# Performance work log

Hardware: AMD Instinct MI355X
Metric: run time of the kernel (lower is better)

The kernel has to match this reference:

```python
import jax, jax.numpy as jnp
import numpy as np

B, T, D, H = 4, 2048, 1024, 16
DH = D // H


def setup_inputs() -> dict:
    key = jax.random.key(0)
    k_x, k_qkv, k_out = jax.random.split(key, 3)
    x = jax.random.normal(k_x, (B, T, D), dtype=jnp.float32)
    padding_mask_1d = jnp.ones((B, T), dtype=bool)
    # Linear weights stored as [in, out] (torch stores [out, in]; math identical via x @ W)
    Wqkv = jax.random.normal(k_qkv, (D, 3 * D), dtype=jnp.float32) * 0.02
    bqkv = jnp.zeros((3 * D,), dtype=jnp.float32)
    Wout = jax.random.normal(k_out, (D, D), dtype=jnp.float32) * 0.02
    bout = jnp.zeros((D,), dtype=jnp.float32)
    return {"x": x, "padding_mask_1d": padding_mask_1d, "Wqkv": Wqkv,
            "bqkv": bqkv, "Wout": Wout, "bout": bout}


def reference(x, padding_mask_1d, Wqkv, bqkv, Wout, bout):
    b, t, d = x.shape
    # QKV projection
    qkv = x @ Wqkv + bqkv                      # [B,T,3D]
    q, k, v = jnp.split(qkv, 3, axis=-1)
    # split heads -> [B,H,T,Dh]
    def split_heads(u):
        return u.reshape(b, t, H, DH).transpose(0, 2, 1, 3)
    Q, K, V = split_heads(q), split_heads(k), split_heads(v)
    # scores [B,H,T,T]
    logits = jnp.einsum('bhqd,bhkd->bhqk', Q, K) / jnp.sqrt(jnp.asarray(DH, x.dtype))
    # padding mask [B,1,1,T] & causal mask [1,1,T,T]
    pad = padding_mask_1d[:, None, None, :]
    causal = jnp.tril(jnp.ones((t, t), dtype=bool))[None, None]
    mask = pad & causal
    logits = jnp.where(mask, logits, -jnp.inf)
    weights = jax.nn.softmax(logits, axis=-1)  # dropout=0.0 -> identity
    out = jnp.einsum('bhqk,bhkd->bhqd', weights, V)  # [B,H,T,Dh]
    out = out.transpose(0, 2, 1, 3).reshape(b, t, d)  # merge heads
    out = out @ Wout + bout
    return out
```

## Files before the change

### kernel.cpp

```cpp
#include <hip/hip_runtime.h>
#include <math.h>

typedef unsigned short u16;
typedef float f32x4 __attribute__((ext_vector_type(4)));
typedef short bf16x8 __attribute__((ext_vector_type(8)));

typedef const unsigned char __attribute__((address_space(1))) cu8_as1;
typedef unsigned char __attribute__((address_space(3))) u8_as3;

__device__ __forceinline__ void gload_lds16(const void* g, void* l) {
  __builtin_amdgcn_global_load_lds((cu8_as1*)g, (u8_as3*)l, 16, 0, 0);
}

__device__ __forceinline__ u16 f2b(float f) {
  union { float f; unsigned u; } v; v.f = f;
  unsigned r = v.u + 0x7FFFu + ((v.u >> 16) & 1u);
  return (u16)(r >> 16);
}

__global__ __launch_bounds__(256) void k_cvt(const float* __restrict__ in,
                                             u16* __restrict__ out, int n4) {
  int i = blockIdx.x * 256 + threadIdx.x;
  if (i >= n4) return;
  float4 v = ((const float4*)in)[i];
  ushort4 o;
  o.x = f2b(v.x); o.y = f2b(v.y); o.z = f2b(v.z); o.w = f2b(v.w);
  ((ushort4*)out)[i] = o;
}

__global__ __launch_bounds__(256) void k_transpose_cvt(const float* __restrict__ in,
                                                       u16* __restrict__ out,
                                                       int R, int C) {
  __shared__ float tile[32][33];
  int c0 = blockIdx.x * 32, r0 = blockIdx.y * 32;
  int tx = threadIdx.x, ty = threadIdx.y;
#pragma unroll
  for (int j = 0; j < 32; j += 8)
    tile[ty + j][tx] = in[(size_t)(r0 + ty + j) * C + c0 + tx];
  __syncthreads();
#pragma unroll
  for (int j = 0; j < 32; j += 8)
    out[(size_t)(c0 + ty + j) * R + r0 + tx] = f2b(tile[tx][ty + j]);
}

#define BM 128
#define BN 128
#define BKk 32

#define QSCALE 0.1803368801111244f

template <int EPI>
__global__ __launch_bounds__(256) void k_gemm_bt(
    const u16* __restrict__ A, const u16* __restrict__ Bt,
    const float* __restrict__ bias, float* __restrict__ outp,
    int M, int N, int K,
    u16* __restrict__ Qb, u16* __restrict__ Kb, u16* __restrict__ Vtb) {
  __shared__ u16 As[BM * BKk];
  __shared__ u16 Bs[BN * BKk];
  int tid = threadIdx.x;
  int lane = tid & 63, w = tid >> 6;
  int lo = lane & 15, hi = lane >> 4;
  int wr = w >> 1, wc = w & 1;
  int m0 = blockIdx.x * BM, n0 = blockIdx.y * BN;
  const u16* Ab = A + (size_t)m0 * K;
  const u16* Bb = Bt + (size_t)n0 * K;

  f32x4 acc[4][4];
#pragma unroll
  for (int i = 0; i < 4; ++i)
#pragma unroll
    for (int j = 0; j < 4; ++j) acc[i][j] = (f32x4){0.f, 0.f, 0.f, 0.f};

  for (int kt = 0; kt < K; kt += BKk) {
#pragma unroll
    for (int q = 0; q < 2; ++q) {
      int idx = q * 256 + tid;
      int row = idx >> 2, cb = idx & 3;
      gload_lds16(Ab + (size_t)row * K + kt + cb * 8, &As[idx * 8]);
      gload_lds16(Bb + (size_t)row * K + kt + cb * 8, &Bs[idx * 8]);
    }
    __syncthreads();
    bf16x8 af[4], bf[4];
#pragma unroll
    for (int i = 0; i < 4; ++i) {
      af[i] = *(const bf16x8*)&As[(wr * 64 + i * 16 + lo) * BKk + hi * 8];
      bf[i] = *(const bf16x8*)&Bs[(wc * 64 + i * 16 + lo) * BKk + hi * 8];
    }
#pragma unroll
    for (int i = 0; i < 4; ++i)
#pragma unroll
      for (int j = 0; j < 4; ++j)
        acc[i][j] = __builtin_amdgcn_mfma_f32_16x16x32_bf16(af[i], bf[j], acc[i][j], 0, 0, 0);
    __syncthreads();
  }

#pragma unroll
  for (int i = 0; i < 4; ++i) {
#pragma unroll
    for (int j = 0; j < 4; ++j) {
      int col = n0 + wc * 64 + j * 16 + lo;
      float bv = bias[col];
#pragma unroll
      for (int r = 0; r < 4; ++r) {
        int row = m0 + wr * 64 + i * 16 + hi * 4 + r;
        float v = acc[i][j][r] + bv;
        if (EPI == 1) {
          outp[(size_t)row * N + col] = v;
        } else {
          int b = row >> 11, t = row & 2047;
          int reg = col >> 10, nr = col & 1023;
          int h = nr >> 6, d = nr & 63;
          int bh = b * 16 + h;
          if (reg == 0)
            Qb[((size_t)bh * 2048 + t) * 64 + d] = f2b(v * QSCALE);
          else if (reg == 1)
            Kb[((size_t)bh * 2048 + t) * 64 + d] = f2b(v);
          else
            Vtb[((size_t)bh * 64 + d) * 2048 + t] = f2b(v);
        }
      }
    }
  }
}

#define M2FIX 8.0f

__global__ __launch_bounds__(128) void k_attn(const u16* __restrict__ Qb,
                                              const u16* __restrict__ Kb,
                                              const u16* __restrict__ Vtb,
                                              u16* __restrict__ Ob) {
  __shared__ u16 Pl[2][32 * 40];
  int lane = threadIdx.x & 63, w = threadIdx.x >> 6;
  int lo = lane & 15, hi = lane >> 4;
  int bh = blockIdx.x;
  int qt = ((gridDim.y - 1 - blockIdx.y) << 1) + w;
  int qr = qt * 32;
  const u16* Qh = Qb + (size_t)bh * 2048 * 64;
  const u16* Kh = Kb + (size_t)bh * 2048 * 64;
  const u16* Vh = Vtb + (size_t)bh * 64 * 2048;
  u16* Pw = Pl[w];

  bf16x8 qf[2][2];
#pragma unroll
  for (int m = 0; m < 2; ++m)
#pragma unroll
    for (int c = 0; c < 2; ++c)
      qf[m][c] = *(const bf16x8*)&Qh[(size_t)(qr + m * 16 + lo) * 64 + c * 32 + hi * 8];

  f32x4 o[2][4];
  float lsum[2][4];
#pragma unroll
  for (int m = 0; m < 2; ++m) {
#pragma unroll
    for (int dc = 0; dc < 4; ++dc) o[m][dc] = (f32x4){0.f, 0.f, 0.f, 0.f};
#pragma unroll
    for (int r = 0; r < 4; ++r) lsum[m][r] = 0.f;
  }

  for (int kt = 0; kt < qr + 32; kt += 32) {
    bf16x8 kf[2][2];
#pragma unroll
    for (int kc = 0; kc < 2; ++kc)
#pragma unroll
      for (int c = 0; c < 2; ++c)
        kf[kc][c] = *(const bf16x8*)&Kh[(size_t)(kt + kc * 16 + lo) * 64 + c * 32 + hi * 8];

    f32x4 s[2][2];
#pragma unroll
    for (int m = 0; m < 2; ++m)
#pragma unroll
      for (int kc = 0; kc < 2; ++kc) {
        f32x4 z = (f32x4){0.f, 0.f, 0.f, 0.f};
        z = __builtin_amdgcn_mfma_f32_16x16x32_bf16(qf[m][0], kf[kc][0], z, 0, 0, 0);
        s[m][kc] = __builtin_amdgcn_mfma_f32_16x16x32_bf16(qf[m][1], kf[kc][1], z, 0, 0, 0);
      }

    if (kt + 31 > qr) {
#pragma unroll
      for (int m = 0; m < 2; ++m)
#pragma unroll
        for (int kc = 0; kc < 2; ++kc) {
          int key = kt + kc * 16 + lo;
#pragma unroll
          for (int r = 0; r < 4; ++r) {
            int rowa = qr + m * 16 + hi * 4 + r;
            if (key > rowa) s[m][kc][r] = -INFINITY;
          }
        }
    }

#pragma unroll
    for (int m = 0; m < 2; ++m) {
#pragma unroll
      for (int kc = 0; kc < 2; ++kc)
#pragma unroll
        for (int r = 0; r < 4; ++r)
          s[m][kc][r] = __builtin_amdgcn_exp2f(s[m][kc][r] - M2FIX);
#pragma unroll
      for (int r = 0; r < 4; ++r)
        lsum[m][r] += s[m][0][r] + s[m][1][r];
#pragma unroll
      for (int kc = 0; kc < 2; ++kc)
#pragma unroll
        for (int r = 0; r < 4; ++r)
          Pw[(m * 16 + hi * 4 + r) * 40 + kc * 16 + lo] = f2b(s[m][kc][r]);
    }

    bf16x8 pa[2];
#pragma unroll
    for (int m = 0; m < 2; ++m)
      pa[m] = *(const bf16x8*)&Pw[(m * 16 + lo) * 40 + hi * 8];
    bf16x8 vf[4];
#pragma unroll
    for (int dc = 0; dc < 4; ++dc)
      vf[dc] = *(const bf16x8*)&Vh[(size_t)(dc * 16 + lo) * 2048 + kt + hi * 8];
#pragma unroll
    for (int m = 0; m < 2; ++m)
#pragma unroll
      for (int dc = 0; dc < 4; ++dc)
        o[m][dc] = __builtin_amdgcn_mfma_f32_16x16x32_bf16(pa[m], vf[dc], o[m][dc], 0, 0, 0);
  }

#pragma unroll
  for (int m = 0; m < 2; ++m)
#pragma unroll
    for (int off = 1; off < 16; off <<= 1)
#pragma unroll
      for (int r = 0; r < 4; ++r)
        lsum[m][r] += __shfl_xor(lsum[m][r], off);

  int b = bh >> 4, h = bh & 15;
#pragma unroll
  for (int m = 0; m < 2; ++m) {
    float rl[4];
#pragma unroll
    for (int r = 0; r < 4; ++r) rl[r] = 1.f / lsum[m][r];
#pragma unroll
    for (int dc = 0; dc < 4; ++dc)
#pragma unroll
      for (int r = 0; r < 4; ++r) {
        int t = qr + m * 16 + hi * 4 + r;
        int d = h * 64 + dc * 16 + lo;
        Ob[((size_t)(b * 2048 + t)) * 1024 + d] = f2b(o[m][dc][r] * rl[r]);
      }
  }
}

extern "C" void kernel_launch(void* const* d_in, const int* in_sizes, int n_in,
                              void* d_out, int out_size, void* d_ws, size_t ws_size,
                              hipStream_t stream) {
  const float* x    = (const float*)d_in[0];
  const float* Wqkv = (const float*)d_in[2];
  const float* bqkv = (const float*)d_in[3];
  const float* Wout = (const float*)d_in[4];
  const float* bout = (const float*)d_in[5];
  float* out = (float*)d_out;

  char* ws = (char*)d_ws;
  u16* xb    = (u16*)(ws);
  u16* WqkvT = (u16*)(ws + (16u << 20));
  u16* WoutT = (u16*)(ws + (22u << 20));
  u16* Qb    = (u16*)(ws + (24u << 20));
  u16* Kb    = (u16*)(ws + (40u << 20));
  u16* Vtb   = (u16*)(ws + (56u << 20));
  u16* Ob    = (u16*)(ws + (72u << 20));

  k_cvt<<<8192, 256, 0, stream>>>(x, xb, 8192 * 1024 / 4);
  k_transpose_cvt<<<dim3(96, 32), dim3(32, 8), 0, stream>>>(Wqkv, WqkvT, 1024, 3072);
  k_transpose_cvt<<<dim3(32, 32), dim3(32, 8), 0, stream>>>(Wout, WoutT, 1024, 1024);
  k_gemm_bt<0><<<dim3(64, 24), 256, 0, stream>>>(xb, WqkvT, bqkv, nullptr,
                                                 8192, 3072, 1024, Qb, Kb, Vtb);
  k_attn<<<dim3(64, 32), 128, 0, stream>>>(Qb, Kb, Vtb, Ob);
  k_gemm_bt<1><<<dim3(64, 8), 256, 0, stream>>>(Ob, WoutT, bout, out,
                                                8192, 1024, 1024, nullptr, nullptr, nullptr);
}
```

Measured before the change: 339.2 us.

## Split attention key range across two waves and combine partial outputs

Each attention block now serves a single 32-row query tile, and its two waves each process half of the causal key tiles instead of separate query tiles. The grid doubles to 64×64 blocks. Each wave writes its unnormalized bf16 partial output and row sums. A new combine kernel adds the two partials and normalizes them. Because the softmax max is fixed, no rescaling is needed when combining. The aim is shorter per-wave critical paths and better balance of the causal tail, at the cost of an extra launch, roughly 48MB of extra traffic, loading Q twice, and extra bf16 rounding of the partial sums.

Result: slower. 350.2 us (+3.2%).

```diff
diff --git a/kernel.cpp b/kernel.cpp
--- a/kernel.cpp
+++ b/kernel.cpp
@@ -16,6 +16,11 @@
   union { float f; unsigned u; } v; v.f = f;
   unsigned r = v.u + 0x7FFFu + ((v.u >> 16) & 1u);
   return (u16)(r >> 16);
+}
+
+__device__ __forceinline__ float b2f(unsigned hi16_at_lo) {
+  union { unsigned u; float f; } v; v.u = hi16_at_lo;
+  return v.f;
 }
 
 __global__ __launch_bounds__(256) void k_cvt(const float* __restrict__ in,
@@ -128,17 +133,22 @@
 __global__ __launch_bounds__(128) void k_attn(const u16* __restrict__ Qb,
                                               const u16* __restrict__ Kb,
                                               const u16* __restrict__ Vtb,
-                                              u16* __restrict__ Ob) {
+                                              u16* __restrict__ Op0,
+                                              u16* __restrict__ Op1,
+                                              float* __restrict__ L0,
+                                              float* __restrict__ L1) {
   __shared__ u16 Pl[2][32 * 40];
-  int lane = threadIdx.x & 63, w = threadIdx.x >> 6;
+  int lane = threadIdx.x & 63, s = threadIdx.x >> 6;
   int lo = lane & 15, hi = lane >> 4;
   int bh = blockIdx.x;
-  int qt = ((gridDim.y - 1 - blockIdx.y) << 1) + w;
+  int qt = 63 - blockIdx.y;
   int qr = qt * 32;
+  int T = qt + 1, ht = T >> 1;
+  int ti0 = s ? ht : 0, ti1 = s ? T : ht;
   const u16* Qh = Qb + (size_t)bh * 2048 * 64;
   const u16* Kh = Kb + (size_t)bh * 2048 * 64;
   const u16* Vh = Vtb + (size_t)bh * 64 * 2048;
-  u16* Pw = Pl[w];
+  u16* Pw = Pl[s];
 
   bf16x8 qf[2][2];
 #pragma unroll
@@ -157,7 +167,8 @@
     for (int r = 0; r < 4; ++r) lsum[m][r] = 0.f;
   }
 
-  for (int kt = 0; kt < qr + 32; kt += 32) {
+  for (int ti = ti0; ti < ti1; ++ti) {
+    int kt = ti * 32;
     bf16x8 kf[2][2];
 #pragma unroll
     for (int kc = 0; kc < 2; ++kc)
@@ -165,14 +176,14 @@
       for (int c = 0; c < 2; ++c)
         kf[kc][c] = *(const bf16x8*)&Kh[(size_t)(kt + kc * 16 + lo) * 64 + c * 32 + hi * 8];
 
-    f32x4 s[2][2];
+    f32x4 sv[2][2];
 #pragma unroll
     for (int m = 0; m < 2; ++m)
 #pragma unroll
       for (int kc = 0; kc < 2; ++kc) {
         f32x4 z = (f32x4){0.f, 0.f, 0.f, 0.f};
         z = __builtin_amdgcn_mfma_f32_16x16x32_bf16(qf[m][0], kf[kc][0], z, 0, 0, 0);
-        s[m][kc] = __builtin_amdgcn_mfma_f32_16x16x32_bf16(qf[m][1], kf[kc][1], z, 0, 0, 0);
+        sv[m][kc] = __builtin_amdgcn_mfma_f32_16x16x32_bf16(qf[m][1], kf[kc][1], z, 0, 0, 0);
       }
 
     if (kt + 31 > qr) {
@@ -184,7 +195,7 @@
 #pragma unroll
           for (int r = 0; r < 4; ++r) {
             int rowa = qr + m * 16 + hi * 4 + r;
-            if (key > rowa) s[m][kc][r] = -INFINITY;
+            if (key > rowa) sv[m][kc][r] = -INFINITY;
           }
         }
     }
@@ -195,15 +206,15 @@
       for (int kc = 0; kc < 2; ++kc)
 #pragma unroll
         for (int r = 0; r < 4; ++r)
-          s[m][kc][r] = __builtin_amdgcn_exp2f(s[m][kc][r] - M2FIX);
+          sv[m][kc][r] = __builtin_amdgcn_exp2f(sv[m][kc][r] - M2FIX);
 #pragma unroll
       for (int r = 0; r < 4; ++r)
-        lsum[m][r] += s[m][0][r] + s[m][1][r];
+        lsum[m][r] += sv[m][0][r] + sv[m][1][r];
 #pragma unroll
       for (int kc = 0; kc < 2; ++kc)
 #pragma unroll
         for (int r = 0; r < 4; ++r)
-          Pw[(m * 16 + hi * 4 + r) * 40 + kc * 16 + lo] = f2b(s[m][kc][r]);
+          Pw[(m * 16 + hi * 4 + r) * 40 + kc * 16 + lo] = f2b(sv[m][kc][r]);
     }
 
     bf16x8 pa[2];
@@ -229,21 +240,52 @@
       for (int r = 0; r < 4; ++r)
         lsum[m][r] += __shfl_xor(lsum[m][r], off);
 
+  u16* Op = s ? Op1 : Op0;
+  float* Lb = s ? L1 : L0;
   int b = bh >> 4, h = bh & 15;
 #pragma unroll
   for (int m = 0; m < 2; ++m) {
-    float rl[4];
-#pragma unroll
-    for (int r = 0; r < 4; ++r) rl[r] = 1.f / lsum[m][r];
 #pragma unroll
     for (int dc = 0; dc < 4; ++dc)
 #pragma unroll
       for (int r = 0; r < 4; ++r) {
         int t = qr + m * 16 + hi * 4 + r;
         int d = h * 64 + dc * 16 + lo;
-        Ob[((size_t)(b * 2048 + t)) * 1024 + d] = f2b(o[m][dc][r] * rl[r]);
+        Op[((size_t)(b * 2048 + t)) * 1024 + d] = f2b(o[m][dc][r]);
       }
-  }
+    if (lo == 0)
+#pragma unroll
+      for (int r = 0; r < 4; ++r)
+        Lb[(size_t)bh * 2048 + qr + m * 16 + hi * 4 + r] = lsum[m][r];
+  }
+}
+
+__global__ __launch_bounds__(256) void k_combine(const u16* __restrict__ Op0,
+                                                 u16* __restrict__ Op1,
+                                                 const float* __restrict__ L0,
+                                                 const float* __restrict__ L1) {
+  int i = blockIdx.x * 256 + threadIdx.x;
+  size_t base = (size_t)i << 3;
+  int row = (int)(base >> 10);
+  int col = (int)(base & 1023);
+  int b = row >> 11, t = row & 2047;
+  int bh = b * 16 + (col >> 6);
+  size_t li = (size_t)bh * 2048 + t;
+  float rl = 1.f / (L0[li] + L1[li]);
+  uint4 a = ((const uint4*)Op0)[i];
+  uint4 c = ((const uint4*)Op1)[i];
+  unsigned av[4] = {a.x, a.y, a.z, a.w};
+  unsigned cv[4] = {c.x, c.y, c.z, c.w};
+  unsigned ov[4];
+#pragma unroll
+  for (int j = 0; j < 4; ++j) {
+    float alo = b2f(av[j] << 16), ahi = b2f(av[j] & 0xffff0000u);
+    float clo = b2f(cv[j] << 16), chi = b2f(cv[j] & 0xffff0000u);
+    unsigned rlo = f2b((alo + clo) * rl);
+    unsigned rhi = f2b((ahi + chi) * rl);
+    ov[j] = rlo | (rhi << 16);
+  }
+  ((uint4*)Op1)[i] = make_uint4(ov[0], ov[1], ov[2], ov[3]);
 }
 
 extern "C" void kernel_launch(void* const* d_in, const int* in_sizes, int n_in,
@@ -263,14 +305,18 @@
   u16* Qb    = (u16*)(ws + (24u << 20));
   u16* Kb    = (u16*)(ws + (40u << 20));
   u16* Vtb   = (u16*)(ws + (56u << 20));
-  u16* Ob    = (u16*)(ws + (72u << 20));
+  u16* Op1   = (u16*)(ws + (72u << 20));
+  u16*   Op0 = (u16*)(ws);
+  float* L0  = (float*)(ws + (16u << 20));
+  float* L1  = (float*)(ws + (17u << 20));
 
   k_cvt<<<8192, 256, 0, stream>>>(x, xb, 8192 * 1024 / 4);
   k_transpose_cvt<<<dim3(96, 32), dim3(32, 8), 0, stream>>>(Wqkv, WqkvT, 1024, 3072);
   k_transpose_cvt<<<dim3(32, 32), dim3(32, 8), 0, stream>>>(Wout, WoutT, 1024, 1024);
   k_gemm_bt<0><<<dim3(64, 24), 256, 0, stream>>>(xb, WqkvT, bqkv, nullptr,
                                                  8192, 3072, 1024, Qb, Kb, Vtb);
-  k_attn<<<dim3(64, 32), 128, 0, stream>>>(Qb, Kb, Vtb, Ob);
-  k_gemm_bt<1><<<dim3(64, 8), 256, 0, stream>>>(Ob, WoutT, bout, out,
+  k_attn<<<dim3(64, 64), 128, 0, stream>>>(Qb, Kb, Vtb, Op0, Op1, L0, L1);
+  k_combine<<<4096, 256, 0, stream>>>(Op0, Op1, L0, L1);
+  k_gemm_bt<1><<<dim3(64, 8), 256, 0, stream>>>(Op1, WoutT, bout, out,
                                                 8192, 1024, 1024, nullptr, nullptr, nullptr);
 }
```
